# Optimization experiments

Measured on AMD Instinct MI355X. Metric: run time of the kernel, lower is better.

## Reference

```python
import jax, jax.numpy as jnp
import numpy as np

IN_F, H1, H2, OUT_F = 16, 512, 1024, 16
N_NODES, N_EDGES = 20000, 160000


def gcn_conv(x, src, dst, W, b, n):
    # PyG GCNConv: add self-loops, symmetric deg^-1/2 normalization,
    # linear transform first, then normalized scatter-add aggregation.
    loop = jnp.arange(n, dtype=src.dtype)
    s = jnp.concatenate([src, loop])
    d = jnp.concatenate([dst, loop])
    deg = jax.ops.segment_sum(jnp.ones(s.shape[0], x.dtype), d, num_segments=n)
    dinv = jnp.where(deg > 0, jax.lax.rsqrt(deg), 0.0)
    h = x @ W                      # [n, out]
    norm = dinv[s] * dinv[d]       # [e]
    msg = h[s] * norm[:, None]     # [e, out]
    return jax.ops.segment_sum(msg, d, num_segments=n) + b


def setup_inputs() -> dict:
    key = jax.random.key(0)
    ks = jax.random.split(key, 8)
    node_matrix = jax.random.normal(ks[0], (N_NODES, IN_F), dtype=jnp.float32)
    graph = jax.random.randint(ks[1], (2, N_EDGES), 0, N_NODES, dtype=jnp.int64)
    def glorot(k, shape):
        lim = np.sqrt(6.0 / (shape[0] + shape[1]))
        return jax.random.uniform(k, shape, jnp.float32, -lim, lim)
    return {
        "node_matrix": node_matrix,
        "graph": graph,
        "W1": glorot(ks[2], (IN_F, H1)),
        "b1": jnp.zeros((H1,), jnp.float32),
        "W2": glorot(ks[3], (H1, H2)),
        "b2": jnp.zeros((H2,), jnp.float32),
        "Wl": glorot(ks[4], (H2, OUT_F)),
        "bl": jnp.zeros((OUT_F,), jnp.float32),
    }


def reference(node_matrix, graph, W1, b1, W2, b2, Wl, bl):
    n = node_matrix.shape[0]
    src, dst = graph[0], graph[1]
    x = gcn_conv(node_matrix, src, dst, W1, b1, n)
    x = jax.nn.relu(x)
    # dropout is identity in eval mode
    x = gcn_conv(x, src, dst, W2, b2, n)
    return x @ Wl + bl
```

## Files before the change

kernel.cpp:

```cpp
#include <hip/hip_runtime.h>


constexpr int IN_F  = 16;
constexpr int H1D   = 512;
constexpr int H2D   = 1024;
constexpr int OUTF  = 16;

__global__ void k_init(float* __restrict__ dinv, float* __restrict__ WfB,
                       float* __restrict__ bf, float* __restrict__ W1T,
                       const float* __restrict__ W1, int n) {
  int t = blockIdx.x * blockDim.x + threadIdx.x;
  if (t < n) dinv[t] = 1.0f;
  if (t < OUTF * H1D) WfB[t] = 0.0f;
  if (t < OUTF) bf[t] = 0.0f;
  if (t < IN_F * H1D) {
    int j = t >> 4, k = t & 15;
    W1T[t] = W1[k * H1D + j];
  }
}

__global__ void k_deg(const int* __restrict__ dst, float* __restrict__ deg, int e) {
  int t = blockIdx.x * blockDim.x + threadIdx.x;
  if (t < e) atomicAdd(&deg[dst[t]], 1.0f);
}

__global__ void k_rsqrt(float* __restrict__ dinv, int n) {
  int t = blockIdx.x * blockDim.x + threadIdx.x;
  if (t < n) dinv[t] = rsqrtf(dinv[t]);
}

__global__ void k_fuseW(const float* __restrict__ W2, const float* __restrict__ Wl,
                        float* __restrict__ WfB) {
  int g = blockIdx.x * blockDim.x + threadIdx.x;
  int o = g & (OUTF - 1);
  int j = (g >> 4) & (H1D - 1);
  int c = g >> 13;
  int k0 = c * (H2D / 8);
  float a0 = 0.f, a1 = 0.f, a2 = 0.f, a3 = 0.f;
  const float* w2r = W2 + (size_t)j * H2D;
  for (int k = k0; k < k0 + H2D / 8; k += 4) {
    a0 = fmaf(w2r[k + 0], Wl[(k + 0) * OUTF + o], a0);
    a1 = fmaf(w2r[k + 1], Wl[(k + 1) * OUTF + o], a1);
    a2 = fmaf(w2r[k + 2], Wl[(k + 2) * OUTF + o], a2);
    a3 = fmaf(w2r[k + 3], Wl[(k + 3) * OUTF + o], a3);
  }
  atomicAdd(&WfB[j * OUTF + o], (a0 + a1) + (a2 + a3));
}

__global__ void k_fuseb(const float* __restrict__ b2, const float* __restrict__ Wl,
                        const float* __restrict__ bl, float* __restrict__ bf) {
  int t = threadIdx.x;
  int o = t & (OUTF - 1);
  int c = t >> 4;
  float acc = (c == 0) ? bl[o] : 0.f;
  for (int k = c * (H2D / 8); k < (c + 1) * (H2D / 8); ++k)
    acc = fmaf(b2[k], Wl[k * OUTF + o], acc);
  atomicAdd(&bf[o], acc);
}

__global__ void k_self(const float* __restrict__ V, const float* __restrict__ dinv,
                       float* __restrict__ O, int n) {
  int t = blockIdx.x * blockDim.x + threadIdx.x;
  if (t < n * 16) {
    int i = t >> 4;
    float dv = dinv[i];
    O[t] = V[t] * dv * dv;
  }
}

__global__ void k_agg(const float* __restrict__ V, const int* __restrict__ src,
                      const int* __restrict__ dst, const float* __restrict__ dinv,
                      float* __restrict__ O, int e) {
  int t = blockIdx.x * blockDim.x + threadIdx.x;
  if (t < e * 16) {
    int ed = t >> 4, k = t & 15;
    int s = src[ed], d = dst[ed];
    float nrm = dinv[s] * dinv[d];
    atomicAdd(&O[d * 16 + k], V[s * 16 + k] * nrm);
  }
}

template <int JC>
__global__ __launch_bounds__(256) void k_mlp_part(const float* __restrict__ Xa,
                                                  const float* __restrict__ W1T,
                                                  const float* __restrict__ b1,
                                                  const float* __restrict__ WfB,
                                                  float* __restrict__ part, int n) {
  int i = blockIdx.x * 256 + threadIdx.x;
  int c = blockIdx.y;
  bool valid = (i < n);
  int is = valid ? i : 0;

  float x[16];
  const float4* xr = (const float4*)(Xa + (size_t)is * 16);
#pragma unroll
  for (int q = 0; q < 4; ++q) {
    float4 v = xr[q];
    x[q * 4 + 0] = v.x; x[q * 4 + 1] = v.y; x[q * 4 + 2] = v.z; x[q * 4 + 3] = v.w;
  }

  float a[16];
#pragma unroll
  for (int o = 0; o < 16; ++o) a[o] = 0.f;

  const float* w1p = W1T + (size_t)c * JC * 16;
  const float* wfp = WfB + (size_t)c * JC * 16;
  const float* b1p = b1 + (size_t)c * JC;

#pragma unroll 4
  for (int jj = 0; jj < JC; ++jj) {
    const float* w1r = w1p + jj * 16;
    const float* wfr = wfp + jj * 16;
    float h0 = b1p[jj], h1 = 0.f, h2 = 0.f, h3 = 0.f;
#pragma unroll
    for (int k = 0; k < 4; ++k) {
      h0 = fmaf(x[k +  0], w1r[k +  0], h0);
      h1 = fmaf(x[k +  4], w1r[k +  4], h1);
      h2 = fmaf(x[k +  8], w1r[k +  8], h2);
      h3 = fmaf(x[k + 12], w1r[k + 12], h3);
    }
    float h = fmaxf((h0 + h1) + (h2 + h3), 0.f);
#pragma unroll
    for (int o = 0; o < 16; ++o) a[o] = fmaf(h, wfr[o], a[o]);
  }

  if (valid) {
    float4* pr = (float4*)(part + ((size_t)c * n + i) * 16);
#pragma unroll
    for (int q = 0; q < 4; ++q)
      pr[q] = make_float4(a[q * 4 + 0], a[q * 4 + 1], a[q * 4 + 2], a[q * 4 + 3]);
  }
}

__global__ void k_comb_self(const float* __restrict__ part, const float* __restrict__ dinv,
                            const float* __restrict__ bf, float* __restrict__ G,
                            float* __restrict__ out, int n, int C) {
  int t = blockIdx.x * blockDim.x + threadIdx.x;
  if (t < n * 4) {
    const float4* p = (const float4*)part;
    size_t stride = (size_t)n * 4;
    float4 s = p[t];
    for (int c = 1; c < C; ++c) {
      float4 v = p[(size_t)c * stride + t];
      s.x += v.x; s.y += v.y; s.z += v.z; s.w += v.w;
    }
    ((float4*)G)[t] = s;
    int i = t >> 2, q = t & 3;
    float dv = dinv[i]; dv *= dv;
    float4 b = ((const float4*)bf)[q];
    float4 o = make_float4(fmaf(s.x, dv, b.x), fmaf(s.y, dv, b.y),
                           fmaf(s.z, dv, b.z), fmaf(s.w, dv, b.w));
    ((float4*)out)[t] = o;
  }
}

extern "C" void kernel_launch(void* const* d_in, const int* in_sizes, int n_in,
                              void* d_out, int out_size, void* d_ws, size_t ws_size,
                              hipStream_t stream) {
  (void)n_in; (void)out_size;
  const float* X   = (const float*)d_in[0];
  const int*   gr  = (const int*)d_in[1];
  const float* W1  = (const float*)d_in[2];
  const float* b1  = (const float*)d_in[3];
  const float* W2  = (const float*)d_in[4];
  const float* b2  = (const float*)d_in[5];
  const float* Wl  = (const float*)d_in[6];
  const float* bl  = (const float*)d_in[7];

  int n = in_sizes[0] / IN_F;
  int e = in_sizes[1] / 2;
  const int* src = gr;
  const int* dst = gr + e;

  float* ws   = (float*)d_ws;
  float* dinv = ws;
  float* Xa   = dinv + n;
  float* G    = Xa + (size_t)n * 16;
  float* WfB  = G + (size_t)n * 16;
  float* bf   = WfB + OUTF * H1D;
  float* W1T  = bf + 16;
  float* part = W1T + IN_F * H1D;
  float* out  = (float*)d_out;

  size_t used = (size_t)(part - ws) * 4;
  int C = 8;
  while (C > 1 && used + (size_t)C * n * 16 * 4 > ws_size) C >>= 1;

  const int TPB = 256;
  int nb_n   = (n + TPB - 1) / TPB;
  int nb_e   = (e + TPB - 1) / TPB;
  int nb_n16 = (n * 16 + TPB - 1) / TPB;
  int nb_e16 = (e * 16 + TPB - 1) / TPB;
  int nb_n4  = (n * 4 + TPB - 1) / TPB;
  int nb_ini = ((n > OUTF * H1D ? n : OUTF * H1D) + TPB - 1) / TPB;

  k_init<<<nb_ini, TPB, 0, stream>>>(dinv, WfB, bf, W1T, W1, n);
  k_deg<<<nb_e, TPB, 0, stream>>>(dst, dinv, e);
  k_rsqrt<<<nb_n, TPB, 0, stream>>>(dinv, n);
  k_fuseW<<<(H1D * OUTF * 8) / TPB, TPB, 0, stream>>>(W2, Wl, WfB);
  k_fuseb<<<1, 128, 0, stream>>>(b2, Wl, bl, bf);

  k_self<<<nb_n16, TPB, 0, stream>>>(X, dinv, Xa, n);
  k_agg<<<nb_e16, TPB, 0, stream>>>(X, src, dst, dinv, Xa, e);

  dim3 mg(nb_n, C);
  switch (C) {
    case 8: k_mlp_part<H1D / 8><<<mg, TPB, 0, stream>>>(Xa, W1T, b1, WfB, part, n); break;
    case 4: k_mlp_part<H1D / 4><<<mg, TPB, 0, stream>>>(Xa, W1T, b1, WfB, part, n); break;
    case 2: k_mlp_part<H1D / 2><<<mg, TPB, 0, stream>>>(Xa, W1T, b1, WfB, part, n); break;
    default: k_mlp_part<H1D><<<mg, TPB, 0, stream>>>(Xa, W1T, b1, WfB, part, n); break;
  }
  k_comb_self<<<nb_n4, TPB, 0, stream>>>(part, dinv, bf, G, out, n, C);

  k_agg<<<nb_e16, TPB, 0, stream>>>(G, src, dst, dinv, out, e);
}
```

Before: 153.5 us.

## Replace atomic scatter aggregation with CSR build and per-node gather

```diff
diff --git a/kernel.cpp b/kernel.cpp
--- a/kernel.cpp
+++ b/kernel.cpp
@@ -6,11 +6,11 @@
 constexpr int H2D   = 1024;
 constexpr int OUTF  = 16;
 
-__global__ void k_init(float* __restrict__ dinv, float* __restrict__ WfB,
-                       float* __restrict__ bf, float* __restrict__ W1T,
-                       const float* __restrict__ W1, int n) {
-  int t = blockIdx.x * blockDim.x + threadIdx.x;
-  if (t < n) dinv[t] = 1.0f;
+__global__ void k_setup(int* __restrict__ counts, float* __restrict__ WfB,
+                        float* __restrict__ bf, float* __restrict__ W1T,
+                        const float* __restrict__ W1, int n) {
+  int t = blockIdx.x * blockDim.x + threadIdx.x;
+  if (t < n) counts[t] = 0;
   if (t < OUTF * H1D) WfB[t] = 0.0f;
   if (t < OUTF) bf[t] = 0.0f;
   if (t < IN_F * H1D) {
@@ -19,65 +19,121 @@
   }
 }
 
-__global__ void k_deg(const int* __restrict__ dst, float* __restrict__ deg, int e) {
-  int t = blockIdx.x * blockDim.x + threadIdx.x;
-  if (t < e) atomicAdd(&deg[dst[t]], 1.0f);
-}
-
-__global__ void k_rsqrt(float* __restrict__ dinv, int n) {
-  int t = blockIdx.x * blockDim.x + threadIdx.x;
-  if (t < n) dinv[t] = rsqrtf(dinv[t]);
-}
-
-__global__ void k_fuseW(const float* __restrict__ W2, const float* __restrict__ Wl,
-                        float* __restrict__ WfB) {
-  int g = blockIdx.x * blockDim.x + threadIdx.x;
-  int o = g & (OUTF - 1);
-  int j = (g >> 4) & (H1D - 1);
-  int c = g >> 13;
-  int k0 = c * (H2D / 8);
-  float a0 = 0.f, a1 = 0.f, a2 = 0.f, a3 = 0.f;
-  const float* w2r = W2 + (size_t)j * H2D;
-  for (int k = k0; k < k0 + H2D / 8; k += 4) {
-    a0 = fmaf(w2r[k + 0], Wl[(k + 0) * OUTF + o], a0);
-    a1 = fmaf(w2r[k + 1], Wl[(k + 1) * OUTF + o], a1);
-    a2 = fmaf(w2r[k + 2], Wl[(k + 2) * OUTF + o], a2);
-    a3 = fmaf(w2r[k + 3], Wl[(k + 3) * OUTF + o], a3);
-  }
-  atomicAdd(&WfB[j * OUTF + o], (a0 + a1) + (a2 + a3));
-}
-
-__global__ void k_fuseb(const float* __restrict__ b2, const float* __restrict__ Wl,
-                        const float* __restrict__ bl, float* __restrict__ bf) {
-  int t = threadIdx.x;
-  int o = t & (OUTF - 1);
-  int c = t >> 4;
-  float acc = (c == 0) ? bl[o] : 0.f;
-  for (int k = c * (H2D / 8); k < (c + 1) * (H2D / 8); ++k)
-    acc = fmaf(b2[k], Wl[k * OUTF + o], acc);
-  atomicAdd(&bf[o], acc);
-}
-
-__global__ void k_self(const float* __restrict__ V, const float* __restrict__ dinv,
-                       float* __restrict__ O, int n) {
-  int t = blockIdx.x * blockDim.x + threadIdx.x;
-  if (t < n * 16) {
-    int i = t >> 4;
-    float dv = dinv[i];
-    O[t] = V[t] * dv * dv;
-  }
-}
-
-__global__ void k_agg(const float* __restrict__ V, const int* __restrict__ src,
-                      const int* __restrict__ dst, const float* __restrict__ dinv,
-                      float* __restrict__ O, int e) {
-  int t = blockIdx.x * blockDim.x + threadIdx.x;
-  if (t < e * 16) {
-    int ed = t >> 4, k = t & 15;
-    int s = src[ed], d = dst[ed];
-    float nrm = dinv[s] * dinv[d];
-    atomicAdd(&O[d * 16 + k], V[s * 16 + k] * nrm);
-  }
+__global__ void k_count(const int* __restrict__ dst, int* __restrict__ counts, int e) {
+  int t = blockIdx.x * blockDim.x + threadIdx.x;
+  if (t < e) atomicAdd(&counts[dst[t]], 1);
+}
+
+__global__ void k_scan_fuse(int* __restrict__ counts, int* __restrict__ row_start,
+                            int* __restrict__ cursor, float* __restrict__ dinv,
+                            const float* __restrict__ W2, const float* __restrict__ Wl,
+                            float* __restrict__ WfB, const float* __restrict__ b2,
+                            const float* __restrict__ bl, float* __restrict__ bf,
+                            int n) {
+  int b = blockIdx.x;
+  int tid = threadIdx.x;
+  if (b == 0) {
+    __shared__ int sbuf[256];
+    __shared__ int scarry;
+    if (tid == 0) scarry = 0;
+    __syncthreads();
+    int ntiles = (n + 255) / 256;
+    for (int tile = 0; tile < ntiles; ++tile) {
+      int idx = tile * 256 + tid;
+      int v = (idx < n) ? counts[idx] : 0;
+      sbuf[tid] = v;
+      __syncthreads();
+#pragma unroll
+      for (int off = 1; off < 256; off <<= 1) {
+        int tv = (tid >= off) ? sbuf[tid - off] : 0;
+        __syncthreads();
+        sbuf[tid] += tv;
+        __syncthreads();
+      }
+      int excl = sbuf[tid] - v;
+      if (idx < n) {
+        int s = scarry + excl;
+        row_start[idx] = s;
+        cursor[idx] = s;
+      }
+      int total = sbuf[255];
+      __syncthreads();
+      if (tid == 0) scarry += total;
+      __syncthreads();
+    }
+  } else if (b <= 256) {
+    int g = (b - 1) * 256 + tid;
+    int o = g & (OUTF - 1);
+    int j = (g >> 4) & (H1D - 1);
+    int c = g >> 13;
+    int k0 = c * (H2D / 8);
+    float a0 = 0.f, a1 = 0.f, a2 = 0.f, a3 = 0.f;
+    const float* w2r = W2 + (size_t)j * H2D;
+    for (int k = k0; k < k0 + H2D / 8; k += 4) {
+      a0 = fmaf(w2r[k + 0], Wl[(k + 0) * OUTF + o], a0);
+      a1 = fmaf(w2r[k + 1], Wl[(k + 1) * OUTF + o], a1);
+      a2 = fmaf(w2r[k + 2], Wl[(k + 2) * OUTF + o], a2);
+      a3 = fmaf(w2r[k + 3], Wl[(k + 3) * OUTF + o], a3);
+    }
+    atomicAdd(&WfB[j * OUTF + o], (a0 + a1) + (a2 + a3));
+  } else if (b == 257) {
+    if (tid < 128) {
+      int o = tid & (OUTF - 1);
+      int c = tid >> 4;
+      float acc = (c == 0) ? bl[o] : 0.f;
+      for (int k = c * (H2D / 8); k < (c + 1) * (H2D / 8); ++k)
+        acc = fmaf(b2[k], Wl[k * OUTF + o], acc);
+      atomicAdd(&bf[o], acc);
+    }
+  } else {
+    int i = (b - 258) * 256 + tid;
+    if (i < n) dinv[i] = rsqrtf(1.0f + (float)counts[i]);
+  }
+}
+
+__global__ void k_fill(const int* __restrict__ src, const int* __restrict__ dst,
+                       int* __restrict__ cursor, int* __restrict__ csr, int e) {
+  int t = blockIdx.x * blockDim.x + threadIdx.x;
+  if (t < e) {
+    int d = dst[t];
+    int slot = atomicAdd(&cursor[d], 1);
+    csr[slot] = src[t];
+  }
+}
+
+__global__ __launch_bounds__(256) void k_gather(const float* __restrict__ V,
+                                                const int* __restrict__ csr,
+                                                const int* __restrict__ row_start,
+                                                const int* __restrict__ counts,
+                                                const float* __restrict__ dinv,
+                                                const float* __restrict__ bias,
+                                                float* __restrict__ O, int n) {
+  int t = blockIdx.x * 256 + threadIdx.x;
+  if (t >= n * 4) return;
+  int i = t >> 2, q = t & 3;
+  float di = dinv[i];
+  int start = row_start[i];
+  int cnt = counts[i];
+  float4 acc = ((const float4*)(V + (size_t)i * 16))[q];
+  acc.x *= di; acc.y *= di; acc.z *= di; acc.w *= di;
+  for (int k = 0; k < cnt; ++k) {
+    int s = csr[start + k];
+    float ds = dinv[s];
+    float4 v = ((const float4*)(V + (size_t)s * 16))[q];
+    acc.x = fmaf(v.x, ds, acc.x);
+    acc.y = fmaf(v.y, ds, acc.y);
+    acc.z = fmaf(v.z, ds, acc.z);
+    acc.w = fmaf(v.w, ds, acc.w);
+  }
+  float4 o;
+  if (bias) {
+    float4 bq = ((const float4*)bias)[q];
+    o = make_float4(fmaf(acc.x, di, bq.x), fmaf(acc.y, di, bq.y),
+                    fmaf(acc.z, di, bq.z), fmaf(acc.w, di, bq.w));
+  } else {
+    o = make_float4(acc.x * di, acc.y * di, acc.z * di, acc.w * di);
+  }
+  ((float4*)O + (size_t)i * 4)[q] = o;
 }
 
 template <int JC>
@@ -132,9 +188,8 @@
   }
 }
 
-__global__ void k_comb_self(const float* __restrict__ part, const float* __restrict__ dinv,
-                            const float* __restrict__ bf, float* __restrict__ G,
-                            float* __restrict__ out, int n, int C) {
+__global__ void k_comb(const float* __restrict__ part, float* __restrict__ G,
+                       int n, int C) {
   int t = blockIdx.x * blockDim.x + threadIdx.x;
   if (t < n * 4) {
     const float4* p = (const float4*)part;
@@ -145,12 +200,6 @@
       s.x += v.x; s.y += v.y; s.z += v.z; s.w += v.w;
     }
     ((float4*)G)[t] = s;
-    int i = t >> 2, q = t & 3;
-    float dv = dinv[i]; dv *= dv;
-    float4 b = ((const float4*)bf)[q];
-    float4 o = make_float4(fmaf(s.x, dv, b.x), fmaf(s.y, dv, b.y),
-                           fmaf(s.z, dv, b.z), fmaf(s.w, dv, b.w));
-    ((float4*)out)[t] = o;
   }
 }
 
@@ -179,29 +228,30 @@
   float* WfB  = G + (size_t)n * 16;
   float* bf   = WfB + OUTF * H1D;
   float* W1T  = bf + 16;
-  float* part = W1T + IN_F * H1D;
+  int*   counts    = (int*)(W1T + IN_F * H1D);
+  int*   row_start = counts + n;
+  int*   cursor    = row_start + n;
+  int*   csr       = cursor + n;
+  float* part      = (float*)(csr + e);
   float* out  = (float*)d_out;
 
-  size_t used = (size_t)(part - ws) * 4;
+  size_t used = (size_t)((char*)part - (char*)ws);
   int C = 8;
   while (C > 1 && used + (size_t)C * n * 16 * 4 > ws_size) C >>= 1;
 
   const int TPB = 256;
   int nb_n   = (n + TPB - 1) / TPB;
   int nb_e   = (e + TPB - 1) / TPB;
-  int nb_n16 = (n * 16 + TPB - 1) / TPB;
-  int nb_e16 = (e * 16 + TPB - 1) / TPB;
   int nb_n4  = (n * 4 + TPB - 1) / TPB;
   int nb_ini = ((n > OUTF * H1D ? n : OUTF * H1D) + TPB - 1) / TPB;
 
-  k_init<<<nb_ini, TPB, 0, stream>>>(dinv, WfB, bf, W1T, W1, n);
-  k_deg<<<nb_e, TPB, 0, stream>>>(dst, dinv, e);
-  k_rsqrt<<<nb_n, TPB, 0, stream>>>(dinv, n);
-  k_fuseW<<<(H1D * OUTF * 8) / TPB, TPB, 0, stream>>>(W2, Wl, WfB);
-  k_fuseb<<<1, 128, 0, stream>>>(b2, Wl, bl, bf);
-
-  k_self<<<nb_n16, TPB, 0, stream>>>(X, dinv, Xa, n);
-  k_agg<<<nb_e16, TPB, 0, stream>>>(X, src, dst, dinv, Xa, e);
+  k_setup<<<nb_ini, TPB, 0, stream>>>(counts, WfB, bf, W1T, W1, n);
+  k_count<<<nb_e, TPB, 0, stream>>>(dst, counts, e);
+  k_scan_fuse<<<258 + nb_n, TPB, 0, stream>>>(counts, row_start, cursor, dinv,
+                                              W2, Wl, WfB, b2, bl, bf, n);
+  k_fill<<<nb_e, TPB, 0, stream>>>(src, dst, cursor, csr, e);
+
+  k_gather<<<nb_n4, TPB, 0, stream>>>(X, csr, row_start, counts, dinv, nullptr, Xa, n);
 
   dim3 mg(nb_n, C);
   switch (C) {
@@ -210,7 +260,7 @@
     case 2: k_mlp_part<H1D / 2><<<mg, TPB, 0, stream>>>(Xa, W1T, b1, WfB, part, n); break;
     default: k_mlp_part<H1D><<<mg, TPB, 0, stream>>>(Xa, W1T, b1, WfB, part, n); break;
   }
-  k_comb_self<<<nb_n4, TPB, 0, stream>>>(part, dinv, bf, G, out, n, C);
-
-  k_agg<<<nb_e16, TPB, 0, stream>>>(G, src, dst, dinv, out, e);
-}
+  k_comb<<<nb_n4, TPB, 0, stream>>>(part, G, n, C);
+
+  k_gather<<<nb_n4, TPB, 0, stream>>>(G, csr, row_start, counts, dinv, bf, out, n);
+}
```

After: 223.7 us. +45.8%, slower.
